# Kernel optimization log

Measured on AMD Instinct MI355X. Metric: run time of the kernel, lower is better.

The kernel has to match this reference:

```python
import jax, jax.numpy as jnp
import numpy as np

NUM_NODES = 10101   # 1 root + 100 supers + 10000 leaves
NUM_LEAVES = 10000
TEMPERATURE = 1.0
# weights from the source: root_weight=0, super_weight=1, leaf_weight=1
PATH_WEIGHTS = np.array([0.0, 1.0, 1.0], dtype=np.float32)
TOTAL_WEIGHT = float(PATH_WEIGHTS.sum())


def setup_inputs() -> dict:
    key = jax.random.key(0)
    k1, k2 = jax.random.split(key)
    features = jax.random.normal(k1, (8192, 128), dtype=jnp.float32)
    prototypes = jax.random.normal(k2, (NUM_NODES, 128), dtype=jnp.float32)
    # hierarchy: leaf i (node id 101+i) -> path [root=0, super=1+i//100, leaf=101+i]
    leaf = np.arange(NUM_LEAVES)
    path_idx = np.stack([np.zeros(NUM_LEAVES, dtype=np.int32),
                         (1 + leaf // 100).astype(np.int32),
                         (101 + leaf).astype(np.int32)], axis=1)  # [L, 3]
    return {"features": features, "prototypes": prototypes,
            "path_idx": jnp.asarray(path_idx)}


def reference(features, prototypes, path_idx):
    # ProCoLoss stand-in: node-level logits [N, num_nodes]
    node_logits = jnp.einsum('nd,cd->nc', features, prototypes) / TEMPERATURE
    # gather 3 path logits per leaf and weighted-sum (replaces per-leaf loop)
    gathered = node_logits[:, path_idx]                      # [N, L, 3]
    w = jnp.asarray(PATH_WEIGHTS)
    leaf_logits = jnp.einsum('nlk,k->nl', gathered, w) / TOTAL_WEIGHT  # [N, L]
    return leaf_logits
```

## Files before the change

### kernel.cpp

```cpp
#include <hip/hip_runtime.h>
#include <hip/hip_bf16.h>
#include <stdint.h>

#define M_DIM      8192
#define K_DIM      128
#define NUM_LEAVES 10000
#define N_PAD      10112
#define NT         79
#define MT         64
#define LDS_STRIDE 136

typedef __attribute__((ext_vector_type(8))) short bf16x8;
typedef __attribute__((ext_vector_type(4))) float f32x4;

static __device__ __forceinline__ unsigned short f2bf(float f) {
    union { float f; uint32_t u; } v; v.f = f;
    uint32_t u = v.u;
    u += 0x7FFFu + ((u >> 16) & 1u);
    return (unsigned short)(u >> 16);
}

__global__ void prep_features(const float* __restrict__ F, unsigned short* __restrict__ Fb) {
    int t = blockIdx.x * blockDim.x + threadIdx.x;
    float4 v = ((const float4*)F)[t];
    ushort4 o;
    o.x = f2bf(v.x); o.y = f2bf(v.y); o.z = f2bf(v.z); o.w = f2bf(v.w);
    ((ushort4*)Fb)[t] = o;
}

__global__ void prep_q(const float* __restrict__ P, const int* __restrict__ idx,
                       unsigned short* __restrict__ Qb) {
    int t = blockIdx.x * blockDim.x + threadIdx.x;
    int l = t >> 5;
    int c = (t & 31) << 2;
    ushort4 o;
    if (l < NUM_LEAVES) {
        int i1 = idx[l * 3 + 1];
        int i2 = idx[l * 3 + 2];
        float4 a = *(const float4*)&P[(size_t)i1 * K_DIM + c];
        float4 b = *(const float4*)&P[(size_t)i2 * K_DIM + c];
        o.x = f2bf(0.5f * (a.x + b.x));
        o.y = f2bf(0.5f * (a.y + b.y));
        o.z = f2bf(0.5f * (a.z + b.z));
        o.w = f2bf(0.5f * (a.w + b.w));
    } else {
        o.x = 0; o.y = 0; o.z = 0; o.w = 0;
    }
    *(ushort4*)&Qb[(size_t)l * K_DIM + c] = o;
}

__global__ __launch_bounds__(256, 2) void gemm_fq(
    const unsigned short* __restrict__ Fb,
    const unsigned short* __restrict__ Qb,
    float* __restrict__ out) {
    __shared__ unsigned short As[128 * LDS_STRIDE];
    __shared__ unsigned short Bs[128 * LDS_STRIDE];

    const int bn = blockIdx.x;
    const int bm = blockIdx.y;
    const int tid = threadIdx.x;

    {
        const uint4* gA = (const uint4*)(Fb + (size_t)bm * 128 * K_DIM);
        const uint4* gB = (const uint4*)(Qb + (size_t)bn * 128 * K_DIM);
#pragma unroll
        for (int i = 0; i < 8; ++i) {
            int c = tid + i * 256;
            int r = c >> 4;
            int c8 = (c & 15) << 3;
            uint4 va = gA[c];
            uint4 vb = gB[c];
            *(uint4*)&As[r * LDS_STRIDE + c8] = va;
            *(uint4*)&Bs[r * LDS_STRIDE + c8] = vb;
        }
    }
    __syncthreads();

    const int lane = tid & 63;
    const int w    = tid >> 6;
    const int wm   = (w >> 1) * 64;
    const int wn   = (w & 1) * 64;
    const int l15  = lane & 15;
    const int quad = lane >> 4;

    f32x4 acc[4][4] = {};

#pragma unroll
    for (int kt = 0; kt < 4; ++kt) {
        const int k0 = kt * 32 + quad * 8;
        bf16x8 af[4], bfr[4];
#pragma unroll
        for (int i = 0; i < 4; ++i) {
            af[i]  = *(const bf16x8*)&As[(wm + i * 16 + l15) * LDS_STRIDE + k0];
            bfr[i] = *(const bf16x8*)&Bs[(wn + i * 16 + l15) * LDS_STRIDE + k0];
        }
#pragma unroll
        for (int mi = 0; mi < 4; ++mi)
#pragma unroll
            for (int ni = 0; ni < 4; ++ni)
                acc[mi][ni] = __builtin_amdgcn_mfma_f32_16x16x32_bf16(
                    af[mi], bfr[ni], acc[mi][ni], 0, 0, 0);
    }

    const int rbase = bm * 128 + wm + quad * 4;
    const int cbase = bn * 128 + wn + l15;
#pragma unroll
    for (int mi = 0; mi < 4; ++mi) {
#pragma unroll
        for (int ni = 0; ni < 4; ++ni) {
            int c = cbase + ni * 16;
            if (c < NUM_LEAVES) {
#pragma unroll
                for (int r = 0; r < 4; ++r) {
                    out[(size_t)(rbase + mi * 16 + r) * NUM_LEAVES + c] = acc[mi][ni][r];
                }
            }
        }
    }
}

extern "C" void kernel_launch(void* const* d_in, const int* in_sizes, int n_in,
                              void* d_out, int out_size, void* d_ws, size_t ws_size,
                              hipStream_t stream) {
    const float* F  = (const float*)d_in[0];
    const float* P  = (const float*)d_in[1];
    const int* idx  = (const int*)d_in[2];
    float* out      = (float*)d_out;

    unsigned short* Fb = (unsigned short*)d_ws;
    unsigned short* Qb = Fb + (size_t)M_DIM * K_DIM;

    prep_features<<<(M_DIM * K_DIM / 4) / 256, 256, 0, stream>>>(F, Fb);
    prep_q<<<(N_PAD * 32) / 256, 256, 0, stream>>>(P, idx, Qb);
    gemm_fq<<<dim3(NT, MT), 256, 0, stream>>>(Fb, Qb, out);
}
```

Measured before the change: 366.8 us.

## Load MFMA operands directly from global and store vectorized nontemporal output

Removes the LDS staging and barrier from the GEMM, so each wave loads its bf16 operand fragments straight from global memory. The operand roles are swapped (leaves as the A side), which gives each lane four consecutive output columns, and these are written as 16-byte nontemporal vector stores instead of scalar strided stores. Occupancy hint raised to 3 blocks. This targets the output-write bound (8192x10000 fp32) and LDS overhead, at the cost of redundant global loads across waves, which should mostly hit in cache.

```diff
diff --git a/kernel.cpp b/kernel.cpp
--- a/kernel.cpp
+++ b/kernel.cpp
@@ -8,7 +8,6 @@
 #define N_PAD      10112
 #define NT         79
 #define MT         64
-#define LDS_STRIDE 136
 
 typedef __attribute__((ext_vector_type(8))) short bf16x8;
 typedef __attribute__((ext_vector_type(4))) float f32x4;
@@ -49,71 +48,50 @@
     *(ushort4*)&Qb[(size_t)l * K_DIM + c] = o;
 }
 
-__global__ __launch_bounds__(256, 2) void gemm_fq(
+__global__ __launch_bounds__(256, 3) void gemm_direct(
     const unsigned short* __restrict__ Fb,
     const unsigned short* __restrict__ Qb,
     float* __restrict__ out) {
-    __shared__ unsigned short As[128 * LDS_STRIDE];
-    __shared__ unsigned short Bs[128 * LDS_STRIDE];
-
-    const int bn = blockIdx.x;
-    const int bm = blockIdx.y;
-    const int tid = threadIdx.x;
-
-    {
-        const uint4* gA = (const uint4*)(Fb + (size_t)bm * 128 * K_DIM);
-        const uint4* gB = (const uint4*)(Qb + (size_t)bn * 128 * K_DIM);
-#pragma unroll
-        for (int i = 0; i < 8; ++i) {
-            int c = tid + i * 256;
-            int r = c >> 4;
-            int c8 = (c & 15) << 3;
-            uint4 va = gA[c];
-            uint4 vb = gB[c];
-            *(uint4*)&As[r * LDS_STRIDE + c8] = va;
-            *(uint4*)&Bs[r * LDS_STRIDE + c8] = vb;
-        }
-    }
-    __syncthreads();
-
+    const int bn   = blockIdx.x;
+    const int bm   = blockIdx.y;
+    const int tid  = threadIdx.x;
     const int lane = tid & 63;
     const int w    = tid >> 6;
-    const int wm   = (w >> 1) * 64;
-    const int wn   = (w & 1) * 64;
+    const int wl   = (w & 1) * 64;
+    const int wn   = (w >> 1) * 64;
     const int l15  = lane & 15;
     const int quad = lane >> 4;
+
+    const unsigned short* Ab = Qb + ((size_t)(bn * 128 + wl + l15)) * K_DIM + quad * 8;
+    const unsigned short* Bb = Fb + ((size_t)(bm * 128 + wn + l15)) * K_DIM + quad * 8;
 
     f32x4 acc[4][4] = {};
 
 #pragma unroll
     for (int kt = 0; kt < 4; ++kt) {
-        const int k0 = kt * 32 + quad * 8;
-        bf16x8 af[4], bfr[4];
+        bf16x8 a[4], b[4];
 #pragma unroll
         for (int i = 0; i < 4; ++i) {
-            af[i]  = *(const bf16x8*)&As[(wm + i * 16 + l15) * LDS_STRIDE + k0];
-            bfr[i] = *(const bf16x8*)&Bs[(wn + i * 16 + l15) * LDS_STRIDE + k0];
+            a[i] = *(const bf16x8*)&Ab[(size_t)i * 16 * K_DIM + kt * 32];
+            b[i] = *(const bf16x8*)&Bb[(size_t)i * 16 * K_DIM + kt * 32];
         }
 #pragma unroll
         for (int mi = 0; mi < 4; ++mi)
 #pragma unroll
             for (int ni = 0; ni < 4; ++ni)
                 acc[mi][ni] = __builtin_amdgcn_mfma_f32_16x16x32_bf16(
-                    af[mi], bfr[ni], acc[mi][ni], 0, 0, 0);
+                    a[mi], b[ni], acc[mi][ni], 0, 0, 0);
     }
 
-    const int rbase = bm * 128 + wm + quad * 4;
-    const int cbase = bn * 128 + wn + l15;
 #pragma unroll
     for (int mi = 0; mi < 4; ++mi) {
+        int l = bn * 128 + wl + mi * 16 + quad * 4;
+        if (l < NUM_LEAVES) {
 #pragma unroll
-        for (int ni = 0; ni < 4; ++ni) {
-            int c = cbase + ni * 16;
-            if (c < NUM_LEAVES) {
-#pragma unroll
-                for (int r = 0; r < 4; ++r) {
-                    out[(size_t)(rbase + mi * 16 + r) * NUM_LEAVES + c] = acc[mi][ni][r];
-                }
+            for (int ni = 0; ni < 4; ++ni) {
+                int n = bm * 128 + wn + ni * 16 + l15;
+                __builtin_nontemporal_store(acc[mi][ni],
+                    (f32x4*)&out[(size_t)n * NUM_LEAVES + l]);
             }
         }
     }
@@ -132,5 +110,5 @@
 
     prep_features<<<(M_DIM * K_DIM / 4) / 256, 256, 0, stream>>>(F, Fb);
     prep_q<<<(N_PAD * 32) / 256, 256, 0, stream>>>(P, idx, Qb);
-    gemm_fq<<<dim3(NT, MT), 256, 0, stream>>>(Fb, Qb, out);
+    gemm_direct<<<dim3(NT, MT), 256, 0, stream>>>(Fb, Qb, out);
 }
```

Result: slower. 374.3 us (+2.1%).
